# Kernel optimization log

Hardware: AMD Instinct MI355X
Metric: run time of the kernel (lower is better)

Reference implementation:

```python
import math
import jax, jax.numpy as jnp
import numpy as np

B, S, D, H = 2, 2048, 1024, 16
HD = D // H  # head_dim = 64


def setup_inputs() -> dict:
    key = jax.random.key(0)
    k1, k2, k3 = jax.random.split(key, 3)
    scale = 0.02
    return {
        "x": jax.random.normal(k1, (B, S, D), dtype=jnp.float32),
        "w_qkv": jax.random.normal(k2, (D, 3 * D), dtype=jnp.float32) * scale,
        "b_qkv": jnp.zeros((3 * D,), dtype=jnp.float32),
        "w_proj": jax.random.normal(k3, (D, D), dtype=jnp.float32) * scale,
        "b_proj": jnp.zeros((D,), dtype=jnp.float32),
    }


def reference(x, w_qkv, b_qkv, w_proj, b_proj):
    bsz, seq_len, d_model = x.shape
    # fused qkv projection: [B,S,3D] -> [3,B,H,S,HD]
    qkv = (x @ w_qkv + b_qkv).reshape(bsz, seq_len, 3, H, HD)
    qkv = jnp.transpose(qkv, (2, 0, 3, 1, 4))
    q, k, v = qkv[0], qkv[1], qkv[2]
    # scores [B,H,S,S]
    scores = jnp.einsum("bhqd,bhkd->bhqk", q, k) / math.sqrt(HD)
    causal = jnp.tril(jnp.ones((seq_len, seq_len), dtype=bool))
    scores = jnp.where(causal[None, None], scores, -jnp.inf)
    probs = jax.nn.softmax(scores, axis=-1)
    # dropout = 0.0 (eval mode)
    context = jnp.einsum("bhqk,bhkd->bhqd", probs, v)
    context = jnp.transpose(context, (0, 2, 1, 3)).reshape(bsz, seq_len, d_model)
    return context @ w_proj + b_proj
```

## Files before the change

### kernel.cpp

```cpp
#include <hip/hip_runtime.h>

#define B_ 2
#define S_ 2048
#define D_ 1024
#define H_ 16
#define HD_ 64
#define M_ (B_*S_)
#define N_QKV (3*D_)

typedef __attribute__((ext_vector_type(8))) short short8;
typedef __attribute__((ext_vector_type(4))) float floatx4;

__device__ __forceinline__ float fast_exp2(float x) {
    return __builtin_amdgcn_exp2f(x);
}

__device__ __forceinline__ unsigned short f2b(float f) {
    union { float f; unsigned int u; } v; v.f = f;
    unsigned int u = v.u;
    u += 0x7FFFu + ((u >> 16) & 1u);
    return (unsigned short)(u >> 16);
}
__device__ __forceinline__ unsigned short f2b_fast(float f) {
    union { float f; unsigned int u; } v; v.f = f;
    return (unsigned short)((v.u + 0x8000u) >> 16);
}

__device__ __forceinline__ void glds16(const unsigned short* g, unsigned short* lds) {
    __builtin_amdgcn_global_load_lds(
        (const __attribute__((address_space(1))) unsigned int*)g,
        (__attribute__((address_space(3))) unsigned int*)lds, 16, 0, 0);
}

__global__ void cast_bf16_kernel(const float* __restrict__ src,
                                 unsigned short* __restrict__ dst, int n) {
    int i = (blockIdx.x * blockDim.x + threadIdx.x) * 4;
    if (i >= n) return;
    float4 f = *(const float4*)(src + i);
    ushort4 o;
    o.x = f2b(f.x); o.y = f2b(f.y); o.z = f2b(f.z); o.w = f2b(f.w);
    *(ushort4*)(dst + i) = o;
}

__global__ void transpose_cast_kernel(const float* __restrict__ W,
                                      unsigned short* __restrict__ Wt,
                                      int rows, int cols) {
    __shared__ float tile[32][33];
    int c0 = blockIdx.x * 32, r0 = blockIdx.y * 32;
    int tx = threadIdx.x, ty = threadIdx.y;
    #pragma unroll
    for (int i = 0; i < 4; ++i)
        tile[ty + i*8][tx] = W[(size_t)(r0 + ty + i*8) * cols + c0 + tx];
    __syncthreads();
    #pragma unroll
    for (int i = 0; i < 4; ++i)
        Wt[(size_t)(c0 + ty + i*8) * rows + r0 + tx] = f2b(tile[tx][ty + i*8]);
}

__global__ void vtrans_kernel(const unsigned short* __restrict__ V,
                              unsigned short* __restrict__ Vt) {
    __shared__ unsigned short L[64][72];
    const int t = threadIdx.x;
    const int s0 = blockIdx.x * 64;
    const int bh = blockIdx.y;
    {
        const int sl = t >> 2;
        const int hc = (t & 3) * 16;
        const unsigned short* src = V + ((size_t)bh * S_ + s0 + sl) * HD_ + hc;
        unsigned short tmp[16];
        *(uint4*)&tmp[0] = *(const uint4*)&src[0];
        *(uint4*)&tmp[8] = *(const uint4*)&src[8];
        #pragma unroll
        for (int j = 0; j < 16; ++j) {
            int r = hc + j;
            int pc = sl ^ (16 * ((r >> 4) & 3));
            L[r][pc] = tmp[j];
        }
    }
    __syncthreads();
    {
        const int hl = t >> 2;
        const int sc = (t & 3) * 16;
        const int g = 16 * ((hl >> 4) & 3);
        unsigned short* dst = Vt + ((size_t)bh * HD_ + hl) * S_ + s0 + sc;
        *(uint4*)&dst[0] = *(const uint4*)&L[hl][(sc ^ g) + 0];
        *(uint4*)&dst[8] = *(const uint4*)&L[hl][(sc ^ g) + 8];
    }
}

__global__ __launch_bounds__(256) void gemm_bt_kernel(
    const unsigned short* __restrict__ A,
    const unsigned short* __restrict__ Bt,
    const float* __restrict__ bias,
    unsigned short* __restrict__ q,
    unsigned short* __restrict__ k_,
    unsigned short* __restrict__ v,
    int Kdim)
{
    __shared__ unsigned short As[128*32];
    __shared__ unsigned short Bs[128*32];

    const int t = threadIdx.x;
    const int lane = t & 63;
    const int w = t >> 6;
    const int wm = w >> 1, wn = w & 1;
    const int quad = lane >> 4, l15 = lane & 15;
    const int bm = blockIdx.y, bn = blockIdx.x;

    const int srow = w*16 + (lane >> 2);
    const int scol = (lane & 3) * 8;

    const unsigned short* gA = A  + (size_t)(bm*128 + srow) * Kdim + scol;
    const unsigned short* gB = Bt + (size_t)(bn*128 + srow) * Kdim + scol;
    const size_t rowstep = (size_t)64 * Kdim;

    unsigned short* lA0 = As + (w*16)*32;
    unsigned short* lA1 = As + (64 + w*16)*32;
    unsigned short* lB0 = Bs + (w*16)*32;
    unsigned short* lB1 = Bs + (64 + w*16)*32;

    floatx4 acc[4][4];
    #pragma unroll
    for (int i = 0; i < 4; ++i)
        #pragma unroll
        for (int j = 0; j < 4; ++j)
            acc[i][j] = (floatx4){0.f, 0.f, 0.f, 0.f};

    for (int k0 = 0; k0 < Kdim; k0 += 32) {
        glds16(gA + k0,           lA0);
        glds16(gA + rowstep + k0, lA1);
        glds16(gB + k0,           lB0);
        glds16(gB + rowstep + k0, lB1);
        __syncthreads();
        short8 af[4], bfr[4];
        #pragma unroll
        for (int i = 0; i < 4; ++i)
            af[i] = *(const short8*)&As[(wm*64 + i*16 + l15)*32 + quad*8];
        #pragma unroll
        for (int j = 0; j < 4; ++j)
            bfr[j] = *(const short8*)&Bs[(wn*64 + j*16 + l15)*32 + quad*8];
        #pragma unroll
        for (int i = 0; i < 4; ++i)
            #pragma unroll
            for (int j = 0; j < 4; ++j)
                acc[i][j] = __builtin_amdgcn_mfma_f32_16x16x32_bf16(af[i], bfr[j], acc[i][j], 0, 0, 0);
        __syncthreads();
    }

    #pragma unroll
    for (int i = 0; i < 4; ++i) {
        #pragma unroll
        for (int j = 0; j < 4; ++j) {
            #pragma unroll
            for (int reg = 0; reg < 4; ++reg) {
                int gm = bm*128 + wm*64 + i*16 + quad*4 + reg;
                int gn = bn*128 + wn*64 + j*16 + l15;
                float val = acc[i][j][reg] + bias[gn];
                int b = gm >> 11, s = gm & (S_ - 1);
                int which = gn >> 10, rem = gn & 1023;
                int h = rem >> 6, hd = rem & 63;
                unsigned short bv = f2b(val);
                size_t idx = ((size_t)(b*H_ + h) * S_ + s) * HD_ + hd;
                if (which == 0)      q[idx]  = bv;
                else if (which == 1) k_[idx] = bv;
                else                 v[idx]  = bv;
            }
        }
    }
}

__global__ __launch_bounds__(256) void gemm_bt64_kernel(
    const unsigned short* __restrict__ A,
    const unsigned short* __restrict__ Bt,
    const float* __restrict__ bias,
    float* __restrict__ outf,
    int Ndim, int Kdim)
{
    __shared__ unsigned short As[128*32];
    __shared__ unsigned short Bs[64*32];

    const int t = threadIdx.x;
    const int lane = t & 63;
    const int w = t >> 6;
    const int quad = lane >> 4, l15 = lane & 15;
    const int bm = blockIdx.y, bn = blockIdx.x;

    const int srow = w*16 + (lane >> 2);
    const int scol = (lane & 3) * 8;

    const unsigned short* gA = A  + (size_t)(bm*128 + srow) * Kdim + scol;
    const unsigned short* gB = Bt + (size_t)(bn*64  + srow) * Kdim + scol;
    const size_t rowstep = (size_t)64 * Kdim;

    unsigned short* lA0 = As + (w*16)*32;
    unsigned short* lA1 = As + (64 + w*16)*32;
    unsigned short* lB0 = Bs + (w*16)*32;

    floatx4 acc[2][4];
    #pragma unroll
    for (int i = 0; i < 2; ++i)
        #pragma unroll
        for (int j = 0; j < 4; ++j)
            acc[i][j] = (floatx4){0.f, 0.f, 0.f, 0.f};

    for (int k0 = 0; k0 < Kdim; k0 += 32) {
        glds16(gA + k0,           lA0);
        glds16(gA + rowstep + k0, lA1);
        glds16(gB + k0,           lB0);
        __syncthreads();
        short8 af[2], bfr[4];
        #pragma unroll
        for (int i = 0; i < 2; ++i)
            af[i] = *(const short8*)&As[(w*32 + i*16 + l15)*32 + quad*8];
        #pragma unroll
        for (int j = 0; j < 4; ++j)
            bfr[j] = *(const short8*)&Bs[(j*16 + l15)*32 + quad*8];
        #pragma unroll
        for (int i = 0; i < 2; ++i)
            #pragma unroll
            for (int j = 0; j < 4; ++j)
                acc[i][j] = __builtin_amdgcn_mfma_f32_16x16x32_bf16(af[i], bfr[j], acc[i][j], 0, 0, 0);
        __syncthreads();
    }

    #pragma unroll
    for (int i = 0; i < 2; ++i) {
        #pragma unroll
        for (int j = 0; j < 4; ++j) {
            #pragma unroll
            for (int reg = 0; reg < 4; ++reg) {
                int gm = bm*128 + w*32 + i*16 + quad*4 + reg;
                int gn = bn*64 + j*16 + l15;
                outf[(size_t)gm * Ndim + gn] = acc[i][j][reg] + bias[gn];
            }
        }
    }
}

__global__ __launch_bounds__(256, 2) void attn_kernel(
    const unsigned short* __restrict__ Q,
    const unsigned short* __restrict__ K,
    const unsigned short* __restrict__ Vt,
    unsigned short* __restrict__ ctx)
{
    __shared__ unsigned short Ks[2][64*64];
    __shared__ unsigned short Vs[2][64*64];
    __shared__ unsigned short Pt[4][2][16][72];

    const int t = threadIdx.x;
    const int lane = t & 63, w = t >> 6;
    const int quad = lane >> 4, l15 = lane & 15;
    const int i = blockIdx.x;
    const int bh = i & 31;
    const int qb = (i < 256) ? (15 - (i >> 5)) : ((i - 256) >> 5);
    const int q0 = qb*128 + w*32;

    const unsigned short* Qh  = Q  + (size_t)bh * S_ * HD_;
    const unsigned short* Kh  = K  + (size_t)bh * S_ * HD_;
    const unsigned short* Vth = Vt + (size_t)bh * HD_ * S_;

    const float SCALE = 0.125f * 1.44269504f;
    const float CBIAS = 12.0f;

    short8 bq[2][2];
    #pragma unroll
    for (int qs = 0; qs < 2; ++qs)
        #pragma unroll
        for (int kk = 0; kk < 2; ++kk)
            bq[qs][kk] = *(const short8*)&Qh[(size_t)(q0 + qs*16 + l15)*HD_ + kk*32 + quad*8];

    floatx4 O[2][4];
    #pragma unroll
    for (int qs = 0; qs < 2; ++qs)
        #pragma unroll
        for (int nb = 0; nb < 4; ++nb)
            O[qs][nb] = (floatx4){0.f,0.f,0.f,0.f};
    float l_i[2] = {0.f, 0.f};

    const int ktend  = 2*qb + 1;
    const int mydiag = 2*qb + (w >> 1);

    const int sr0 = t >> 3, sg0 = t & 7;
    auto stage = [&](int kt, int d) {
        #pragma unroll
        for (int ii = 0; ii < 2; ++ii) {
            int r = sr0 + ii*32;
            int g = sg0 ^ (r & 7);
            glds16(Kh + (size_t)(kt*64 + r)*HD_ + g*8, &Ks[d][(w*8 + ii*32)*64]);
            glds16(Vth + (size_t)r*S_ + kt*64 + g*8,   &Vs[d][(w*8 + ii*32)*64]);
        }
    };

    stage(0, 0);

    for (int kt = 0; kt <= ktend; ++kt) {
        const int d = kt & 1;
        __syncthreads();
        if (kt < ktend) stage(kt + 1, d ^ 1);

        if (kt <= mydiag) {
            short8 ak[4][2], av[4][2];
            #pragma unroll
            for (int nb = 0; nb < 4; ++nb)
                #pragma unroll
                for (int kk = 0; kk < 2; ++kk) {
                    int off = (nb*16 + l15)*64 + (((quad + 4*kk) ^ (l15 & 7)) * 8);
                    ak[nb][kk] = *(const short8*)&Ks[d][off];
                    av[nb][kk] = *(const short8*)&Vs[d][off];
                }

            float z[2][4][4];
            #pragma unroll
            for (int qs = 0; qs < 2; ++qs)
                #pragma unroll
                for (int nb = 0; nb < 4; ++nb) {
                    floatx4 c = (floatx4){0.f,0.f,0.f,0.f};
                    c = __builtin_amdgcn_mfma_f32_16x16x32_bf16(ak[nb][0], bq[qs][0], c, 0,0,0);
                    c = __builtin_amdgcn_mfma_f32_16x16x32_bf16(ak[nb][1], bq[qs][1], c, 0,0,0);
                    #pragma unroll
                    for (int r = 0; r < 4; ++r)
                        z[qs][nb][r] = c[r] * SCALE - CBIAS;
                }

            if (kt == mydiag) {
                const int koff = kt * 64;
                #pragma unroll
                for (int qs = 0; qs < 2; ++qs) {
                    int qg = q0 + qs*16 + l15;
                    #pragma unroll
                    for (int nb = 0; nb < 4; ++nb)
                        #pragma unroll
                        for (int r = 0; r < 4; ++r)
                            if (koff + nb*16 + quad*4 + r > qg) z[qs][nb][r] = -1e30f;
                }
            }

            #pragma unroll
            for (int qs = 0; qs < 2; ++qs) {
                float rs = 0.f;
                #pragma unroll
                for (int nb = 0; nb < 4; ++nb) {
                    float p0 = fast_exp2(z[qs][nb][0]);
                    float p1 = fast_exp2(z[qs][nb][1]);
                    float p2 = fast_exp2(z[qs][nb][2]);
                    float p3 = fast_exp2(z[qs][nb][3]);
                    rs += (p0 + p1) + (p2 + p3);
                    ushort4 pk;
                    pk.x = f2b_fast(p0); pk.y = f2b_fast(p1);
                    pk.z = f2b_fast(p2); pk.w = f2b_fast(p3);
                    *(ushort4*)&Pt[w][qs][l15][nb*16 + quad*4] = pk;
                }
                l_i[qs] += rs;
            }

            #pragma unroll
            for (int qs = 0; qs < 2; ++qs) {
                short8 bp0 = *(const short8*)&Pt[w][qs][l15][quad*8];
                short8 bp1 = *(const short8*)&Pt[w][qs][l15][32 + quad*8];
                #pragma unroll
                for (int nb = 0; nb < 4; ++nb) {
                    O[qs][nb] = __builtin_amdgcn_mfma_f32_16x16x32_bf16(av[nb][0], bp0, O[qs][nb], 0,0,0);
                    O[qs][nb] = __builtin_amdgcn_mfma_f32_16x16x32_bf16(av[nb][1], bp1, O[qs][nb], 0,0,0);
                }
            }
        }
    }

    #pragma unroll
    for (int qs = 0; qs < 2; ++qs) {
        l_i[qs] += __shfl_xor(l_i[qs], 16, 64);
        l_i[qs] += __shfl_xor(l_i[qs], 32, 64);
    }

    const int b = bh >> 4, h = bh & (H_ - 1);
    #pragma unroll
    for (int qs = 0; qs < 2; ++qs) {
        float inv = 1.f / l_i[qs];
        int qg = q0 + qs*16 + l15;
        #pragma unroll
        for (int nb = 0; nb < 4; ++nb) {
            ushort4 o;
            o.x = f2b(O[qs][nb][0] * inv);
            o.y = f2b(O[qs][nb][1] * inv);
            o.z = f2b(O[qs][nb][2] * inv);
            o.w = f2b(O[qs][nb][3] * inv);
            *(ushort4*)&ctx[((size_t)(b*S_ + qg))*D_ + h*HD_ + nb*16 + quad*4] = o;
        }
    }
}

extern "C" void kernel_launch(void* const* d_in, const int* in_sizes, int n_in,
                              void* d_out, int out_size, void* d_ws, size_t ws_size,
                              hipStream_t stream) {
    const float* x      = (const float*)d_in[0];
    const float* w_qkv  = (const float*)d_in[1];
    const float* b_qkv  = (const float*)d_in[2];
    const float* w_proj = (const float*)d_in[3];
    const float* b_proj = (const float*)d_in[4];
    float* out = (float*)d_out;

    unsigned short* xb     = (unsigned short*)d_ws;
    unsigned short* wqkvT  = xb     + (size_t)M_ * D_;
    unsigned short* wprojT = wqkvT  + (size_t)N_QKV * D_;
    unsigned short* Qb     = wprojT + (size_t)D_ * D_;
    unsigned short* Kb     = Qb     + (size_t)B_*H_*S_*HD_;
    unsigned short* Vb     = Kb     + (size_t)B_*H_*S_*HD_;
    unsigned short* Vtb    = Vb     + (size_t)B_*H_*S_*HD_;
    unsigned short* ctx    = xb;

    cast_bf16_kernel<<<dim3((M_*D_/4 + 255)/256), dim3(256), 0, stream>>>(x, xb, M_*D_);
    transpose_cast_kernel<<<dim3(N_QKV/32, D_/32), dim3(32, 8), 0, stream>>>(w_qkv, wqkvT, D_, N_QKV);
    transpose_cast_kernel<<<dim3(D_/32, D_/32), dim3(32, 8), 0, stream>>>(w_proj, wprojT, D_, D_);

    gemm_bt_kernel<<<dim3(N_QKV/128, M_/128), dim3(256), 0, stream>>>(
        xb, wqkvT, b_qkv, Qb, Kb, Vb, D_);

    vtrans_kernel<<<dim3(S_/64, B_*H_), dim3(256), 0, stream>>>(Vb, Vtb);

    attn_kernel<<<dim3(512), dim3(256), 0, stream>>>(Qb, Kb, Vtb, ctx);

    gemm_bt64_kernel<<<dim3(D_/64, M_/128), dim3(256), 0, stream>>>(
        ctx, wprojT, b_proj, out, D_, D_);
}
```

Baseline: 192.6 us.

## Pair causal query tiles per block and split KV range across two wave groups

The attention kernel now launches 256 blocks of 512 threads. Each block processes a long and a short causal query tile (qb and 15-qb) one after the other, which balances the per-block work. Within a block, two groups of four waves each take alternate KV tiles, using a 4-deep shared-memory ring. Their partial outputs and row sums are then combined through shared memory before normalisation. This is meant to remove tail imbalance and raise parallelism. The cost is extra shared memory, more barriers and a combine step.

Result: faster. 186.2 us (-3.3%).

```diff
diff --git a/kernel.cpp b/kernel.cpp
--- a/kernel.cpp
+++ b/kernel.cpp
@@ -237,23 +237,23 @@
     }
 }
 
-__global__ __launch_bounds__(256, 2) void attn_kernel(
+__global__ __launch_bounds__(512) void attn_kernel(
     const unsigned short* __restrict__ Q,
     const unsigned short* __restrict__ K,
     const unsigned short* __restrict__ Vt,
     unsigned short* __restrict__ ctx)
 {
-    __shared__ unsigned short Ks[2][64*64];
-    __shared__ unsigned short Vs[2][64*64];
-    __shared__ unsigned short Pt[4][2][16][72];
+    __shared__ unsigned short KVs[4][2][64*64];
+    __shared__ unsigned short Pt[8][2][16][72];
+    __shared__ float Comb[4][64][37];
 
     const int t = threadIdx.x;
     const int lane = t & 63, w = t >> 6;
+    const int g = w & 3, p = w >> 2;
     const int quad = lane >> 4, l15 = lane & 15;
-    const int i = blockIdx.x;
-    const int bh = i & 31;
-    const int qb = (i < 256) ? (15 - (i >> 5)) : ((i - 256) >> 5);
-    const int q0 = qb*128 + w*32;
+    const int bh = blockIdx.x & 31;
+    const int pairi = blockIdx.x >> 5;
+    const int qbA = 15 - pairi, qbB = pairi;
 
     const unsigned short* Qh  = Q  + (size_t)bh * S_ * HD_;
     const unsigned short* Kh  = K  + (size_t)bh * S_ * HD_;
@@ -262,131 +262,163 @@
     const float SCALE = 0.125f * 1.44269504f;
     const float CBIAS = 12.0f;
 
-    short8 bq[2][2];
-    #pragma unroll
-    for (int qs = 0; qs < 2; ++qs)
-        #pragma unroll
-        for (int kk = 0; kk < 2; ++kk)
-            bq[qs][kk] = *(const short8*)&Qh[(size_t)(q0 + qs*16 + l15)*HD_ + kk*32 + quad*8];
-
-    floatx4 O[2][4];
-    #pragma unroll
-    for (int qs = 0; qs < 2; ++qs)
-        #pragma unroll
-        for (int nb = 0; nb < 4; ++nb)
-            O[qs][nb] = (floatx4){0.f,0.f,0.f,0.f};
-    float l_i[2] = {0.f, 0.f};
-
-    const int ktend  = 2*qb + 1;
-    const int mydiag = 2*qb + (w >> 1);
-
-    const int sr0 = t >> 3, sg0 = t & 7;
-    auto stage = [&](int kt, int d) {
-        #pragma unroll
-        for (int ii = 0; ii < 2; ++ii) {
-            int r = sr0 + ii*32;
-            int g = sg0 ^ (r & 7);
-            glds16(Kh + (size_t)(kt*64 + r)*HD_ + g*8, &Ks[d][(w*8 + ii*32)*64]);
-            glds16(Vth + (size_t)r*S_ + kt*64 + g*8,   &Vs[d][(w*8 + ii*32)*64]);
-        }
+    const int TA = 2*qbA + 2;
+    const int TT = TA + 2*qbB + 2;
+
+    const int sr = t >> 3, sc = t & 7;
+    const int gch = sc ^ (sr & 7);
+
+    auto stage_abs = [&](int a) {
+        if (a >= TT) return;
+        int j = (a < TA) ? a : a - TA;
+        int d = a & 3;
+        glds16(Kh  + (size_t)(j*64 + sr)*HD_ + gch*8, &KVs[d][0][(w*8)*64]);
+        glds16(Vth + (size_t)sr*S_ + j*64 + gch*8,    &KVs[d][1][(w*8)*64]);
     };
 
-    stage(0, 0);
-
-    for (int kt = 0; kt <= ktend; ++kt) {
-        const int d = kt & 1;
-        __syncthreads();
-        if (kt < ktend) stage(kt + 1, d ^ 1);
-
-        if (kt <= mydiag) {
-            short8 ak[4][2], av[4][2];
+    auto run_qtile = [&](int qb, int toff) {
+        const int q0 = qb*128 + g*32;
+        const int mydiag = 2*qb + (g >> 1);
+
+        short8 bq[2][2];
+        #pragma unroll
+        for (int qs = 0; qs < 2; ++qs)
+            #pragma unroll
+            for (int kk = 0; kk < 2; ++kk)
+                bq[qs][kk] = *(const short8*)&Qh[(size_t)(q0 + qs*16 + l15)*HD_ + kk*32 + quad*8];
+
+        floatx4 O[2][4];
+        #pragma unroll
+        for (int qs = 0; qs < 2; ++qs)
             #pragma unroll
             for (int nb = 0; nb < 4; ++nb)
-                #pragma unroll
-                for (int kk = 0; kk < 2; ++kk) {
-                    int off = (nb*16 + l15)*64 + (((quad + 4*kk) ^ (l15 & 7)) * 8);
-                    ak[nb][kk] = *(const short8*)&Ks[d][off];
-                    av[nb][kk] = *(const short8*)&Vs[d][off];
-                }
-
-            float z[2][4][4];
-            #pragma unroll
-            for (int qs = 0; qs < 2; ++qs)
-                #pragma unroll
-                for (int nb = 0; nb < 4; ++nb) {
-                    floatx4 c = (floatx4){0.f,0.f,0.f,0.f};
-                    c = __builtin_amdgcn_mfma_f32_16x16x32_bf16(ak[nb][0], bq[qs][0], c, 0,0,0);
-                    c = __builtin_amdgcn_mfma_f32_16x16x32_bf16(ak[nb][1], bq[qs][1], c, 0,0,0);
-                    #pragma unroll
-                    for (int r = 0; r < 4; ++r)
-                        z[qs][nb][r] = c[r] * SCALE - CBIAS;
-                }
-
-            if (kt == mydiag) {
-                const int koff = kt * 64;
-                #pragma unroll
-                for (int qs = 0; qs < 2; ++qs) {
-                    int qg = q0 + qs*16 + l15;
-                    #pragma unroll
-                    for (int nb = 0; nb < 4; ++nb)
+                O[qs][nb] = (floatx4){0.f,0.f,0.f,0.f};
+        float l_i[2] = {0.f, 0.f};
+
+        for (int ph = 0; ph <= qb; ++ph) {
+            __syncthreads();
+            stage_abs(toff + 2*ph + 2);
+            stage_abs(toff + 2*ph + 3);
+
+            const int j = 2*ph + p;
+            if (j <= mydiag) {
+                const int d = (toff + j) & 3;
+                const unsigned short* Ksb = &KVs[d][0][0];
+                const unsigned short* Vsb = &KVs[d][1][0];
+
+                short8 ak[4][2], av[4][2];
+                #pragma unroll
+                for (int nb = 0; nb < 4; ++nb)
+                    #pragma unroll
+                    for (int kk = 0; kk < 2; ++kk) {
+                        int off = (nb*16 + l15)*64 + (((quad + 4*kk) ^ (l15 & 7)) * 8);
+                        ak[nb][kk] = *(const short8*)&Ksb[off];
+                        av[nb][kk] = *(const short8*)&Vsb[off];
+                    }
+
+                float z[2][4][4];
+                #pragma unroll
+                for (int qs = 0; qs < 2; ++qs)
+                    #pragma unroll
+                    for (int nb = 0; nb < 4; ++nb) {
+                        floatx4 c = (floatx4){0.f,0.f,0.f,0.f};
+                        c = __builtin_amdgcn_mfma_f32_16x16x32_bf16(ak[nb][0], bq[qs][0], c, 0,0,0);
+                        c = __builtin_amdgcn_mfma_f32_16x16x32_bf16(ak[nb][1], bq[qs][1], c, 0,0,0);
                         #pragma unroll
                         for (int r = 0; r < 4; ++r)
-                            if (koff + nb*16 + quad*4 + r > qg) z[qs][nb][r] = -1e30f;
+                            z[qs][nb][r] = c[r] * SCALE - CBIAS;
+                    }
+
+                if (j == mydiag) {
+                    const int koff = j * 64;
+                    #pragma unroll
+                    for (int qs = 0; qs < 2; ++qs) {
+                        int qg = q0 + qs*16 + l15;
+                        #pragma unroll
+                        for (int nb = 0; nb < 4; ++nb)
+                            #pragma unroll
+                            for (int r = 0; r < 4; ++r)
+                                if (koff + nb*16 + quad*4 + r > qg) z[qs][nb][r] = -1e30f;
+                    }
                 }
-            }
-
+
+                #pragma unroll
+                for (int qs = 0; qs < 2; ++qs) {
+                    float rs = 0.f;
+                    #pragma unroll
+                    for (int nb = 0; nb < 4; ++nb) {
+                        float p0 = fast_exp2(z[qs][nb][0]);
+                        float p1 = fast_exp2(z[qs][nb][1]);
+                        float p2 = fast_exp2(z[qs][nb][2]);
+                        float p3 = fast_exp2(z[qs][nb][3]);
+                        rs += (p0 + p1) + (p2 + p3);
+                        ushort4 pk;
+                        pk.x = f2b_fast(p0); pk.y = f2b_fast(p1);
+                        pk.z = f2b_fast(p2); pk.w = f2b_fast(p3);
+                        *(ushort4*)&Pt[w][qs][l15][nb*16 + quad*4] = pk;
+                    }
+                    l_i[qs] += rs;
+                }
+
+                #pragma unroll
+                for (int qs = 0; qs < 2; ++qs) {
+                    short8 bp0 = *(const short8*)&Pt[w][qs][l15][quad*8];
+                    short8 bp1 = *(const short8*)&Pt[w][qs][l15][32 + quad*8];
+                    #pragma unroll
+                    for (int nb = 0; nb < 4; ++nb) {
+                        O[qs][nb] = __builtin_amdgcn_mfma_f32_16x16x32_bf16(av[nb][0], bp0, O[qs][nb], 0,0,0);
+                        O[qs][nb] = __builtin_amdgcn_mfma_f32_16x16x32_bf16(av[nb][1], bp1, O[qs][nb], 0,0,0);
+                    }
+                }
+            }
+        }
+
+        if (p == 1) {
             #pragma unroll
             for (int qs = 0; qs < 2; ++qs) {
-                float rs = 0.f;
+                #pragma unroll
+                for (int nb = 0; nb < 4; ++nb)
+                    #pragma unroll
+                    for (int r = 0; r < 4; ++r)
+                        Comb[g][lane][qs*16 + nb*4 + r] = O[qs][nb][r];
+                Comb[g][lane][32 + qs] = l_i[qs];
+            }
+        }
+        __syncthreads();
+        if (p == 0) {
+            #pragma unroll
+            for (int qs = 0; qs < 2; ++qs) {
+                #pragma unroll
+                for (int nb = 0; nb < 4; ++nb)
+                    #pragma unroll
+                    for (int r = 0; r < 4; ++r)
+                        O[qs][nb][r] += Comb[g][lane][qs*16 + nb*4 + r];
+                l_i[qs] += Comb[g][lane][32 + qs];
+                l_i[qs] += __shfl_xor(l_i[qs], 16, 64);
+                l_i[qs] += __shfl_xor(l_i[qs], 32, 64);
+            }
+            const int b = bh >> 4, h = bh & (H_ - 1);
+            #pragma unroll
+            for (int qs = 0; qs < 2; ++qs) {
+                float inv = 1.f / l_i[qs];
+                int qg = q0 + qs*16 + l15;
                 #pragma unroll
                 for (int nb = 0; nb < 4; ++nb) {
-                    float p0 = fast_exp2(z[qs][nb][0]);
-                    float p1 = fast_exp2(z[qs][nb][1]);
-                    float p2 = fast_exp2(z[qs][nb][2]);
-                    float p3 = fast_exp2(z[qs][nb][3]);
-                    rs += (p0 + p1) + (p2 + p3);
-                    ushort4 pk;
-                    pk.x = f2b_fast(p0); pk.y = f2b_fast(p1);
-                    pk.z = f2b_fast(p2); pk.w = f2b_fast(p3);
-                    *(ushort4*)&Pt[w][qs][l15][nb*16 + quad*4] = pk;
+                    ushort4 o;
+                    o.x = f2b(O[qs][nb][0] * inv);
+                    o.y = f2b(O[qs][nb][1] * inv);
+                    o.z = f2b(O[qs][nb][2] * inv);
+                    o.w = f2b(O[qs][nb][3] * inv);
+                    *(ushort4*)&ctx[((size_t)(b*S_ + qg))*D_ + h*HD_ + nb*16 + quad*4] = o;
                 }
-                l_i[qs] += rs;
-            }
-
-            #pragma unroll
-            for (int qs = 0; qs < 2; ++qs) {
-                short8 bp0 = *(const short8*)&Pt[w][qs][l15][quad*8];
-                short8 bp1 = *(const short8*)&Pt[w][qs][l15][32 + quad*8];
-                #pragma unroll
-                for (int nb = 0; nb < 4; ++nb) {
-                    O[qs][nb] = __builtin_amdgcn_mfma_f32_16x16x32_bf16(av[nb][0], bp0, O[qs][nb], 0,0,0);
-                    O[qs][nb] = __builtin_amdgcn_mfma_f32_16x16x32_bf16(av[nb][1], bp1, O[qs][nb], 0,0,0);
-                }
-            }
-        }
-    }
-
-    #pragma unroll
-    for (int qs = 0; qs < 2; ++qs) {
-        l_i[qs] += __shfl_xor(l_i[qs], 16, 64);
-        l_i[qs] += __shfl_xor(l_i[qs], 32, 64);
-    }
-
-    const int b = bh >> 4, h = bh & (H_ - 1);
-    #pragma unroll
-    for (int qs = 0; qs < 2; ++qs) {
-        float inv = 1.f / l_i[qs];
-        int qg = q0 + qs*16 + l15;
-        #pragma unroll
-        for (int nb = 0; nb < 4; ++nb) {
-            ushort4 o;
-            o.x = f2b(O[qs][nb][0] * inv);
-            o.y = f2b(O[qs][nb][1] * inv);
-            o.z = f2b(O[qs][nb][2] * inv);
-            o.w = f2b(O[qs][nb][3] * inv);
-            *(ushort4*)&ctx[((size_t)(b*S_ + qg))*D_ + h*HD_ + nb*16 + quad*4] = o;
-        }
-    }
+            }
+        }
+    };
+
+    stage_abs(0);
+    stage_abs(1);
+    run_qtile(qbA, 0);
+    run_qtile(qbB, TA);
 }
 
 extern "C" void kernel_launch(void* const* d_in, const int* in_sizes, int n_in,
@@ -417,7 +449,7 @@
 
     vtrans_kernel<<<dim3(S_/64, B_*H_), dim3(256), 0, stream>>>(Vb, Vtb);
 
-    attn_kernel<<<dim3(512), dim3(256), 0, stream>>>(Qb, Kb, Vtb, ctx);
+    attn_kernel<<<dim3(256), dim3(512), 0, stream>>>(Qb, Kb, Vtb, ctx);
 
     gemm_bt64_kernel<<<dim3(D_/64, M_/128), dim3(256), 0, stream>>>(
         ctx, wprojT, b_proj, out, D_, D_);
```
